# Kernel tuning notes

Measured on AMD Instinct MI355X. Metric: run time of the kernel, lower is better.

Reference implementation:

```python
import jax, jax.numpy as jnp
import numpy as np

BUCKET_SIZE = 64
LOOK_BACKWARD = 1
LOOK_FORWARD = 0  # causal => no look forward
CAUSAL = True


def look_around(x, backward, forward, pad_value):
    # x: [b, buckets, bucket_size, ...]; pads along the bucket axis and concats
    # shifted windows along the intra-bucket axis (dim=2), matching torch look_around.
    t = x.shape[1]
    pad_cfg = ((0, 0), (backward, forward)) + ((0, 0),) * (x.ndim - 2)
    padded = jnp.pad(x, pad_cfg, constant_values=pad_value)
    return jnp.concatenate([padded[:, i:i + t] for i in range(forward + backward + 1)], axis=2)


def setup_inputs() -> dict:
    key = jax.random.key(0)
    kq, kk, kv = jax.random.split(key, 3)
    shape = (4, 16, 4096, 64)  # [batch, heads, seq, head_dim]
    q = jax.random.normal(kq, shape, dtype=jnp.float32)
    k = jax.random.normal(kk, shape, dtype=jnp.float32)
    v = jax.random.normal(kv, shape, dtype=jnp.float32)
    return {"q": q, "k": k, "v": v}


def reference(q, k, v):
    shape = q.shape
    # merge batch and heads
    merge = lambda t: t.reshape(-1, t.shape[-2], t.shape[-1])
    q, k, v = merge(q), merge(k), merge(v)
    b, t, e = q.shape
    assert t % BUCKET_SIZE == 0
    buckets = t // BUCKET_SIZE

    ticker = jnp.arange(t, dtype=jnp.int32)[None, :]          # [1, t]
    b_t = ticker.reshape(1, buckets, BUCKET_SIZE)              # [1, buckets, bucket]

    bucket_fn = lambda x: x.reshape(b, buckets, BUCKET_SIZE, e)
    bq, bk, bv = bucket_fn(q), bucket_fn(k), bucket_fn(v)

    bk = look_around(bk, LOOK_BACKWARD, LOOK_FORWARD, 0.0)
    bv = look_around(bv, LOOK_BACKWARD, LOOK_FORWARD, 0.0)
    bq_t = b_t                                                 # query positions
    bq_k = look_around(b_t, LOOK_BACKWARD, LOOK_FORWARD, -1)   # key positions, -1 = pad

    scale = e ** (-0.5)
    dots = jnp.einsum('bnie,bnje->bnij', bq, bk) * scale
    mask_value = -jnp.finfo(dots.dtype).max

    if CAUSAL:
        causal_mask = bq_t[:, :, :, None] < bq_k[:, :, None, :]
        dots = jnp.where(causal_mask, mask_value, dots)

    pad_mask = bq_k[:, :, None, :] == -1
    dots = jnp.where(pad_mask, mask_value, dots)

    attn = jax.nn.softmax(dots, axis=-1)
    out = jnp.einsum('bnij,bnje->bnie', attn, bv)
    return out.reshape(shape)
```

## Files before the change

### kernel.cpp

```cpp
#include <hip/hip_runtime.h>
#include <hip/hip_bf16.h>

typedef __attribute__((ext_vector_type(8))) __bf16 bf16x8;
typedef __attribute__((ext_vector_type(2))) __bf16 bf16x2;
typedef __attribute__((ext_vector_type(4))) float f32x4;

#define SEQ   4096
#define HDIM  64
#define BKT   64

__device__ __forceinline__ unsigned pk2(float a, float b) {
    bf16x2 t;
    t[0] = (__bf16)a;
    t[1] = (__bf16)b;
    return __builtin_bit_cast(unsigned, t);
}
__device__ __forceinline__ int swzV(int row) {
    return ((row & 7) ^ ((row >> 3) & 7)) << 4;
}

__global__ void __launch_bounds__(256, 4) local_attn_kernel(
    const float* __restrict__ q, const float* __restrict__ k,
    const float* __restrict__ v, float* __restrict__ out)
{
    __shared__ __align__(16) unsigned short sK[128 * 64];
    __shared__ __align__(16) unsigned short sVt[64 * 128];

    const int tid = threadIdx.x;
    const int bid0 = blockIdx.x;
    const int lg = (bid0 & 7) * 512 + (bid0 >> 3);
    const int bh = lg >> 6;
    const int bucket = lg & 63;

    const int qoff = (bh * SEQ + bucket * BKT) * HDIM;
    const int koff = qoff - BKT * HDIM;
    const int fix0 = (bucket == 0) ? (BKT * HDIM) : 0;

    const int lane = tid & 63;
    const int wid  = tid >> 6;
    const int g = lane >> 4, m = lane & 15;
    const int g4 = g * 4;
    const int qbase = wid * 16;

    char* const sKb = reinterpret_cast<char*>(sK);
    char* const sVb = reinterpret_cast<char*>(sVt);

    f32x4 kreg[8], vreg[8], qreg[4];
    #pragma unroll
    for (int i = 0; i < 8; ++i) {
        const float* p = k + koff + ((i < 4) ? fix0 : 0) + i * 1024 + tid * 4;
        asm volatile("global_load_dwordx4 %0, %1, off"
                     : "=v"(kreg[i]) : "v"(p) : "memory");
    }
    #pragma unroll
    for (int i = 0; i < 8; ++i) {
        const int kb = i * 16 + wid * 4;
        const float* p = v + koff + ((i < 4) ? fix0 : 0) + (kb + g) * HDIM + m * 4;
        asm volatile("global_load_dwordx4 %0, %1, off"
                     : "=v"(vreg[i]) : "v"(p) : "memory");
    }
    #pragma unroll
    for (int h = 0; h < 2; ++h) {
        const float* qp = q + qoff + (qbase + m) * HDIM + h * 32 + g * 8;
        asm volatile("global_load_dwordx4 %0, %1, off"
                     : "=v"(qreg[2 * h]) : "v"(qp) : "memory");
        asm volatile("global_load_dwordx4 %0, %1, off"
                     : "=v"(qreg[2 * h + 1]) : "v"(qp + 4) : "memory");
    }

    asm volatile("s_waitcnt vmcnt(12)" ::: "memory");
    __builtin_amdgcn_sched_barrier(0);
    #pragma unroll
    for (int i = 0; i < 8; ++i) {
        const int flat = i * 1024 + tid * 4;
        const int row = flat >> 6, col = flat & 63;
        uint2 p;
        p.x = pk2(kreg[i][0], kreg[i][1]);
        p.y = pk2(kreg[i][2], kreg[i][3]);
        const int byte = (row * 128 + col * 2) ^ ((row & 7) << 4);
        *reinterpret_cast<uint2*>(sKb + byte) = p;
    }

    asm volatile("s_waitcnt vmcnt(4)" ::: "memory");
    __builtin_amdgcn_sched_barrier(0);
    const int sdx = g & 1;
    const unsigned selG = sdx ? 0x03020706u : 0x05040100u;
    #pragma unroll
    for (int i = 0; i < 8; ++i) {
        const int kb = i * 16 + wid * 4;
        const f32x4 f = vreg[i];
        const unsigned P0 = pk2(f[0], f[1]);
        const unsigned P1 = pk2(f[2], f[3]);
        const unsigned own  = (g < 2) ? P0 : P1;
        const unsigned send = (g < 2) ? P1 : P0;
        const unsigned R = __shfl_xor(send, 32);
        const unsigned T = __shfl_xor(own, 16);
        const unsigned U = __shfl_xor(R, 16);
        const unsigned A0 = (g < 2) ? own : R;
        const unsigned A1 = (g < 2) ? T : U;
        const unsigned A2 = (g < 2) ? R : own;
        const unsigned A3 = (g < 2) ? U : T;
        const unsigned G0 = __builtin_amdgcn_perm(A1, A0, selG);
        const unsigned G1 = __builtin_amdgcn_perm(A3, A2, selG);
        const int er = m * 4 + g;
        const int byte = (er * 256 + kb * 2) ^ swzV(er);
        uint2 p; p.x = G0; p.y = G1;
        *reinterpret_cast<uint2*>(sVb + byte) = p;
    }

    asm volatile("s_waitcnt vmcnt(0)" ::: "memory");
    __builtin_amdgcn_sched_barrier(0);
    const float scale = 0.125f * 1.44269504f;
    bf16x8 bq[2];
    #pragma unroll
    for (int h = 0; h < 2; ++h) {
        uint4 u;
        u.x = pk2(qreg[2 * h][0] * scale, qreg[2 * h][1] * scale);
        u.y = pk2(qreg[2 * h][2] * scale, qreg[2 * h][3] * scale);
        u.z = pk2(qreg[2 * h + 1][0] * scale, qreg[2 * h + 1][1] * scale);
        u.w = pk2(qreg[2 * h + 1][2] * scale, qreg[2 * h + 1][3] * scale);
        bq[h] = __builtin_bit_cast(bf16x8, u);
    }
    __syncthreads();

    f32x4 acc[8];
    #pragma unroll
    for (int c = 0; c < 8; ++c) acc[c] = (f32x4){0.f, 0.f, 0.f, 0.f};
    __builtin_amdgcn_s_setprio(1);
    #pragma unroll
    for (int c = 0; c < 8; ++c) {
        const int krow = c * 16 + m;
        #pragma unroll
        for (int h = 0; h < 2; ++h) {
            const int byte = (krow * 128 + h * 64 + g * 16) ^ ((m & 7) << 4);
            const bf16x8 ak = *reinterpret_cast<const bf16x8*>(sKb + byte);
            acc[c] = __builtin_amdgcn_mfma_f32_16x16x32_bf16(ak, bq[h], acc[c], 0, 0, 0);
        }
    }
    __builtin_amdgcn_s_setprio(0);

    const int qb = qbase + m;
    float mx = -3e38f;
    #pragma unroll
    for (int c = 0; c < 8; ++c) {
        #pragma unroll
        for (int r = 0; r < 4; ++r) {
            const int kk = c * 16 + g4 + r;
            const bool dead = (c >= 4) ? (kk - 64 > qb) : (bucket == 0);
            const float s = dead ? -1e30f : acc[c][r];
            acc[c][r] = s;
            mx = fmaxf(mx, s);
        }
    }
    mx = fmaxf(mx, __shfl_xor(mx, 16));
    mx = fmaxf(mx, __shfl_xor(mx, 32));
    float sum = 0.f;
    uint2 pb[8];
    #pragma unroll
    for (int c = 0; c < 8; ++c) {
        const float p0 = __builtin_amdgcn_exp2f(acc[c][0] - mx);
        const float p1 = __builtin_amdgcn_exp2f(acc[c][1] - mx);
        const float p2 = __builtin_amdgcn_exp2f(acc[c][2] - mx);
        const float p3 = __builtin_amdgcn_exp2f(acc[c][3] - mx);
        sum += (p0 + p1) + (p2 + p3);
        pb[c].x = pk2(p0, p1);
        pb[c].y = pk2(p2, p3);
    }
    sum += __shfl_xor(sum, 16);
    sum += __shfl_xor(sum, 32);
    const float rl = 1.0f / sum;

    const int l0 = m + ((g & 1) << 5);
    const int l1 = l0 + 16;
    const bool hi2 = (g >> 1) != 0;
    bf16x8 bp[4];
    #pragma unroll
    for (int kt = 0; kt < 4; ++kt) {
        const unsigned a0x = __shfl(pb[2 * kt].x, l0),     a0y = __shfl(pb[2 * kt].y, l0);
        const unsigned a1x = __shfl(pb[2 * kt + 1].x, l0), a1y = __shfl(pb[2 * kt + 1].y, l0);
        const unsigned b0x = __shfl(pb[2 * kt].x, l1),     b0y = __shfl(pb[2 * kt].y, l1);
        const unsigned b1x = __shfl(pb[2 * kt + 1].x, l1), b1y = __shfl(pb[2 * kt + 1].y, l1);
        uint4 u;
        u.x = hi2 ? a1x : a0x;
        u.y = hi2 ? a1y : a0y;
        u.z = hi2 ? b1x : b0x;
        u.w = hi2 ? b1y : b0y;
        bp[kt] = __builtin_bit_cast(bf16x8, u);
    }

    f32x4 oacc[4];
    #pragma unroll
    for (int et = 0; et < 4; ++et) oacc[et] = (f32x4){0.f, 0.f, 0.f, 0.f};
    __builtin_amdgcn_s_setprio(1);
    #pragma unroll
    for (int et = 0; et < 4; ++et) {
        const int row = et * 16 + m;
        #pragma unroll
        for (int kt = 0; kt < 4; ++kt) {
            const int byte = (row * 256 + kt * 64 + g * 16) ^ swzV(row);
            const bf16x8 av = *reinterpret_cast<const bf16x8*>(sVb + byte);
            oacc[et] = __builtin_amdgcn_mfma_f32_16x16x32_bf16(av, bp[kt], oacc[et], 0, 0, 0);
        }
    }
    __builtin_amdgcn_s_setprio(0);

    const int qrow = qbase + m;
    #pragma unroll
    for (int et = 0; et < 4; ++et) {
        f32x4 o = oacc[et];
        o[0] *= rl; o[1] *= rl; o[2] *= rl; o[3] *= rl;
        *reinterpret_cast<float4*>(out + qoff + qrow * HDIM + et * 16 + g4) =
            *reinterpret_cast<float4*>(&o);
    }
}

extern "C" void kernel_launch(void* const* d_in, const int* in_sizes, int n_in,
                              void* d_out, int out_size, void* d_ws, size_t ws_size,
                              hipStream_t stream) {
    const float* q = (const float*)d_in[0];
    const float* k = (const float*)d_in[1];
    const float* v = (const float*)d_in[2];
    float* out = (float*)d_out;
    const int bh = in_sizes[0] / (SEQ * HDIM);
    const int nblocks = bh * (SEQ / BKT);
    hipLaunchKernelGGL(local_attn_kernel, dim3(nblocks), dim3(256), 0, stream,
                       q, k, v, out);
}
```

Baseline: 44.83 us.

## Process two query buckets per block sharing a three-bucket K/V window

Each 512-thread block now computes two adjacent query buckets, loading a shared three-bucket K/V window into LDS instead of two buckets per single-bucket block. This removes redundant global reads of K and V across neighboring buckets. In exchange it uses larger LDS and blocks, which can lower occupancy, and launches half as many blocks.

Result: slower. 51.26 us (+14.3%).

```diff
diff --git a/kernel.cpp b/kernel.cpp
--- a/kernel.cpp
+++ b/kernel.cpp
@@ -19,60 +19,63 @@
     return ((row & 7) ^ ((row >> 3) & 7)) << 4;
 }
 
-__global__ void __launch_bounds__(256, 4) local_attn_kernel(
+__global__ void __launch_bounds__(512, 4) local_attn_kernel(
     const float* __restrict__ q, const float* __restrict__ k,
     const float* __restrict__ v, float* __restrict__ out)
 {
-    __shared__ __align__(16) unsigned short sK[128 * 64];
-    __shared__ __align__(16) unsigned short sVt[64 * 128];
+    __shared__ __align__(16) unsigned short sK[192 * 64];
+    __shared__ __align__(16) unsigned short sVt[64 * 192];
 
     const int tid = threadIdx.x;
-    const int bid0 = blockIdx.x;
-    const int lg = (bid0 & 7) * 512 + (bid0 >> 3);
-    const int bh = lg >> 6;
-    const int bucket = lg & 63;
-
-    const int qoff = (bh * SEQ + bucket * BKT) * HDIM;
-    const int koff = qoff - BKT * HDIM;
-    const int fix0 = (bucket == 0) ? (BKT * HDIM) : 0;
+    const int bid = blockIdx.x;
+    const int lg = (bid & 7) * 256 + (bid >> 3);
+    const int bh = lg >> 5;
+    const int t  = lg & 31;
+    const int base = bh * SEQ * HDIM;
+    const int winoff = base + (t * 2 - 1) * BKT * HDIM;
 
     const int lane = tid & 63;
     const int wid  = tid >> 6;
+    const int isB  = wid >> 2;
+    const int wq   = wid & 3;
     const int g = lane >> 4, m = lane & 15;
     const int g4 = g * 4;
-    const int qbase = wid * 16;
+    const int qbase = wq * 16;
+    const int qoffW = base + (t * 2 + isB) * BKT * HDIM;
 
     char* const sKb = reinterpret_cast<char*>(sK);
     char* const sVb = reinterpret_cast<char*>(sVt);
 
-    f32x4 kreg[8], vreg[8], qreg[4];
-    #pragma unroll
-    for (int i = 0; i < 8; ++i) {
-        const float* p = k + koff + ((i < 4) ? fix0 : 0) + i * 1024 + tid * 4;
+    f32x4 kreg[6], vreg[6], qreg[4];
+    #pragma unroll
+    for (int i = 0; i < 6; ++i) {
+        const int fix = (t == 0 && i < 2) ? (BKT * HDIM) : 0;
+        const float* p = k + winoff + fix + i * 2048 + tid * 4;
         asm volatile("global_load_dwordx4 %0, %1, off"
                      : "=v"(kreg[i]) : "v"(p) : "memory");
     }
     #pragma unroll
-    for (int i = 0; i < 8; ++i) {
-        const int kb = i * 16 + wid * 4;
-        const float* p = v + koff + ((i < 4) ? fix0 : 0) + (kb + g) * HDIM + m * 4;
+    for (int i = 0; i < 6; ++i) {
+        const int fix = (t == 0 && i < 2) ? (BKT * HDIM) : 0;
+        const int kb = i * 32 + wid * 4;
+        const float* p = v + winoff + fix + (kb + g) * HDIM + m * 4;
         asm volatile("global_load_dwordx4 %0, %1, off"
                      : "=v"(vreg[i]) : "v"(p) : "memory");
     }
     #pragma unroll
     for (int h = 0; h < 2; ++h) {
-        const float* qp = q + qoff + (qbase + m) * HDIM + h * 32 + g * 8;
+        const float* qp = q + qoffW + (qbase + m) * HDIM + h * 32 + g * 8;
         asm volatile("global_load_dwordx4 %0, %1, off"
                      : "=v"(qreg[2 * h]) : "v"(qp) : "memory");
         asm volatile("global_load_dwordx4 %0, %1, off"
                      : "=v"(qreg[2 * h + 1]) : "v"(qp + 4) : "memory");
     }
 
-    asm volatile("s_waitcnt vmcnt(12)" ::: "memory");
+    asm volatile("s_waitcnt vmcnt(10)" ::: "memory");
     __builtin_amdgcn_sched_barrier(0);
     #pragma unroll
-    for (int i = 0; i < 8; ++i) {
-        const int flat = i * 1024 + tid * 4;
+    for (int i = 0; i < 6; ++i) {
+        const int flat = i * 2048 + tid * 4;
         const int row = flat >> 6, col = flat & 63;
         uint2 p;
         p.x = pk2(kreg[i][0], kreg[i][1]);
@@ -86,8 +89,8 @@
     const int sdx = g & 1;
     const unsigned selG = sdx ? 0x03020706u : 0x05040100u;
     #pragma unroll
-    for (int i = 0; i < 8; ++i) {
-        const int kb = i * 16 + wid * 4;
+    for (int i = 0; i < 6; ++i) {
+        const int kb = i * 32 + wid * 4;
         const f32x4 f = vreg[i];
         const unsigned P0 = pk2(f[0], f[1]);
         const unsigned P1 = pk2(f[2], f[3]);
@@ -103,7 +106,7 @@
         const unsigned G0 = __builtin_amdgcn_perm(A1, A0, selG);
         const unsigned G1 = __builtin_amdgcn_perm(A3, A2, selG);
         const int er = m * 4 + g;
-        const int byte = (er * 256 + kb * 2) ^ swzV(er);
+        const int byte = (er * 384 + kb * 2) ^ swzV(er);
         uint2 p; p.x = G0; p.y = G1;
         *reinterpret_cast<uint2*>(sVb + byte) = p;
     }
@@ -123,13 +126,14 @@
     }
     __syncthreads();
 
+    const int wbase = isB * 64;
     f32x4 acc[8];
     #pragma unroll
     for (int c = 0; c < 8; ++c) acc[c] = (f32x4){0.f, 0.f, 0.f, 0.f};
     __builtin_amdgcn_s_setprio(1);
     #pragma unroll
     for (int c = 0; c < 8; ++c) {
-        const int krow = c * 16 + m;
+        const int krow = wbase + c * 16 + m;
         #pragma unroll
         for (int h = 0; h < 2; ++h) {
             const int byte = (krow * 128 + h * 64 + g * 16) ^ ((m & 7) << 4);
@@ -140,13 +144,14 @@
     __builtin_amdgcn_s_setprio(0);
 
     const int qb = qbase + m;
+    const bool dead_prev = (isB == 0) && (t == 0);
     float mx = -3e38f;
     #pragma unroll
     for (int c = 0; c < 8; ++c) {
         #pragma unroll
         for (int r = 0; r < 4; ++r) {
             const int kk = c * 16 + g4 + r;
-            const bool dead = (c >= 4) ? (kk - 64 > qb) : (bucket == 0);
+            const bool dead = (c >= 4) ? (kk - 64 > qb) : dead_prev;
             const float s = dead ? -1e30f : acc[c][r];
             acc[c][r] = s;
             mx = fmaxf(mx, s);
@@ -197,7 +202,8 @@
         const int row = et * 16 + m;
         #pragma unroll
         for (int kt = 0; kt < 4; ++kt) {
-            const int byte = (row * 256 + kt * 64 + g * 16) ^ swzV(row);
+            const int col = wbase + kt * 32 + g * 8;
+            const int byte = (row * 384 + col * 2) ^ swzV(row);
             const bf16x8 av = *reinterpret_cast<const bf16x8*>(sVb + byte);
             oacc[et] = __builtin_amdgcn_mfma_f32_16x16x32_bf16(av, bp[kt], oacc[et], 0, 0, 0);
         }
@@ -209,7 +215,7 @@
     for (int et = 0; et < 4; ++et) {
         f32x4 o = oacc[et];
         o[0] *= rl; o[1] *= rl; o[2] *= rl; o[3] *= rl;
-        *reinterpret_cast<float4*>(out + qoff + qrow * HDIM + et * 16 + g4) =
+        *reinterpret_cast<float4*>(out + qoffW + qrow * HDIM + et * 16 + g4) =
             *reinterpret_cast<float4*>(&o);
     }
 }
@@ -222,7 +228,7 @@
     const float* v = (const float*)d_in[2];
     float* out = (float*)d_out;
     const int bh = in_sizes[0] / (SEQ * HDIM);
-    const int nblocks = bh * (SEQ / BKT);
-    hipLaunchKernelGGL(local_attn_kernel, dim3(nblocks), dim3(256), 0, stream,
+    const int nblocks = bh * (SEQ / BKT / 2);
+    hipLaunchKernelGGL(local_attn_kernel, dim3(nblocks), dim3(512), 0, stream,
                        q, k, v, out);
 }
```
